# Optimization experiments

Hardware: AMD Instinct MI355X
Metric: run time of the kernel (lower is better)

Reference implementation:

```python
import jax, jax.numpy as jnp
import numpy as np

B, N, C, DK, TOPK = 4, 4096, 256, 64, 8


def setup_inputs() -> dict:
    key = jax.random.key(0)
    k1, k2, k3 = jax.random.split(key, 3)
    x = jax.random.normal(k1, (B, N, C), dtype=jnp.float32)
    # nn.Linear(channels, d_k, bias=False) weights, stored as [C, DK] for x @ W
    W_q = jax.random.normal(k2, (C, DK), dtype=jnp.float32) * (C ** -0.5)
    W_k = jax.random.normal(k3, (C, DK), dtype=jnp.float32) * (C ** -0.5)
    return {"x": x, "W_q": W_q, "W_k": W_k, "top_k": TOPK}


def reference(x, W_q, W_k, top_k):
    d_k = W_q.shape[-1]
    scale = d_k ** -0.5
    Q = x @ W_q                                   # [B, N, DK]
    K = x @ W_k                                   # [B, N, DK]
    S = jnp.einsum('bnd,bmd->bnm', Q, K) * scale  # [B, N, N]
    _, topk_idx = jax.lax.top_k(S, top_k)         # [B, N, top_k]
    n = S.shape[-1]
    # scatter True at top-k column indices per row (mirrors torch scatter_)
    row_mask = lambda idx: jnp.zeros((n,), dtype=bool).at[idx].set(True)
    mask = jax.vmap(jax.vmap(row_mask))(topk_idx)  # [B, N, N] bool
    S_masked = jnp.where(mask, S, -jnp.inf)
    A = jax.nn.softmax(S_masked, axis=-1)
    return A
```

## Files before the change

### kernel.cpp

```cpp
#include <hip/hip_runtime.h>
#include <math.h>

#define NROW 16384
#define NCOL 4096
#define CDIM 256
#define DKDIM 64
#define SCALE 0.125f

typedef float v4f __attribute__((ext_vector_type(4)));

__global__ __launch_bounds__(512, 2) void qk_proj(
    const float* __restrict__ x, const float* __restrict__ Wq,
    const float* __restrict__ Wk, float* __restrict__ Qt,
    float* __restrict__ Kt) {
  __shared__ float4 xs4[64][65];
  const int t = threadIdx.x;
  const int rb = blockIdx.x;
  {
    const float4* xg = (const float4*)(x + (size_t)rb * 64 * CDIM);
    #pragma unroll
    for (int i = 0; i < 8; ++i) {
      int idx = i * 512 + t;
      xs4[idx >> 6][idx & 63] = xg[idx];
    }
  }
  __syncthreads();

  const int lane = t & 63;
  const int wu = __builtin_amdgcn_readfirstlane(t >> 6);
  const int proj = wu >> 2;
  const int chunk = wu & 3;
  const float* __restrict__ Wp = proj ? Wk : Wq;

  float acc[16];
  #pragma unroll
  for (int j = 0; j < 16; ++j) acc[j] = 0.f;

  #pragma unroll 4
  for (int cs = 0; cs < 64; ++cs) {
    float4 xv = xs4[lane][cs];
    const float xc[4] = {xv.x, xv.y, xv.z, xv.w};
    #pragma unroll
    for (int i = 0; i < 4; ++i) {
      const float4* __restrict__ w4 =
          (const float4*)(Wp + (size_t)(cs * 4 + i) * DKDIM + chunk * 16);
      float4 wa = w4[0], wb = w4[1], wc = w4[2], wd = w4[3];
      float xi = xc[i];
      acc[0]  = fmaf(xi, wa.x, acc[0]);  acc[1]  = fmaf(xi, wa.y, acc[1]);
      acc[2]  = fmaf(xi, wa.z, acc[2]);  acc[3]  = fmaf(xi, wa.w, acc[3]);
      acc[4]  = fmaf(xi, wb.x, acc[4]);  acc[5]  = fmaf(xi, wb.y, acc[5]);
      acc[6]  = fmaf(xi, wb.z, acc[6]);  acc[7]  = fmaf(xi, wb.w, acc[7]);
      acc[8]  = fmaf(xi, wc.x, acc[8]);  acc[9]  = fmaf(xi, wc.y, acc[9]);
      acc[10] = fmaf(xi, wc.z, acc[10]); acc[11] = fmaf(xi, wc.w, acc[11]);
      acc[12] = fmaf(xi, wd.x, acc[12]); acc[13] = fmaf(xi, wd.y, acc[13]);
      acc[14] = fmaf(xi, wd.z, acc[14]); acc[15] = fmaf(xi, wd.w, acc[15]);
    }
  }

  const int gr = rb * 64 + lane;
  const int b = gr >> 12;
  const int n = gr & 4095;
  float4* __restrict__ Out4 = (float4*)(proj ? Kt : Qt);
  #pragma unroll
  for (int i = 0; i < 4; ++i) {
    int dg = chunk * 4 + i;
    float4 o = {acc[4 * i], acc[4 * i + 1], acc[4 * i + 2], acc[4 * i + 3]};
    Out4[(size_t)(b * 16 + dg) * 4096 + n] = o;
  }
}

__global__ __launch_bounds__(256, 4) void s_topk(
    const float* __restrict__ Qt, const float* __restrict__ Kt,
    float* __restrict__ out, float* __restrict__ wsv, int* __restrict__ wsi) {
  __shared__ float smem[8448];
  float4* qs = (float4*)smem;
  float (*cv)[33] = (float(*)[33])smem;
  int   (*ci)[33] = (int(*)[33])(smem + 128 * 33);

  const int t = threadIdx.x;
  const int f = blockIdx.x;
  const int slot = f & 7;
  const int i5 = f >> 3;
  const int cl = i5 >> 5;
  const int rbL = i5 & 31;
  const int combo = slot * 4 + cl;
  const int b = combo >> 3;
  const int chunk = combo & 7;
  const int lane = t & 63;
  const int wu = __builtin_amdgcn_readfirstlane(t >> 6);
  const int n0 = rbL * 128;

  const float4* __restrict__ Qt4 = (const float4*)Qt;
  #pragma unroll
  for (int i = 0; i < 8; ++i) {
    int idx = i * 256 + t;
    int g = idx >> 7, row = idx & 127;
    qs[g * 128 + row] = Qt4[(size_t)(b * 16 + g) * 4096 + n0 + row];
  }
  __syncthreads();

  {
    v4f z = {0.f, 0.f, 0.f, 0.f};
    v4f* o4 = (v4f*)out + (size_t)(b * 4096 + n0) * 1024 + chunk * 128;
    #pragma unroll 8
    for (int i = 0; i < 64; ++i) {
      int g = i * 256 + t;
      __builtin_nontemporal_store(z, &o4[(size_t)(g >> 7) * 1024 + (g & 127)]);
    }
  }

  const float4* __restrict__ Kt4 = (const float4*)Kt;
  const int stripe = chunk * 512 + wu * 128;

  float tv0[8], tv1[8]; int ti0[8], ti1[8];
  float tmin0, tmin1; int tmpos0, tmpos1;

  auto compute8 = [&](int cb, float* a0, float* a1) {
    #pragma unroll
    for (int j = 0; j < 8; ++j) { a0[j] = 0.f; a1[j] = 0.f; }
    #pragma unroll 2
    for (int g = 0; g < 16; ++g) {
      float4 qa = qs[g * 128 + lane];
      float4 qb = qs[g * 128 + 64 + lane];
      const float4* __restrict__ kg =
          Kt4 + (size_t)(b * 16 + g) * 4096 + cb;
      #pragma unroll
      for (int j = 0; j < 8; ++j) {
        float4 kf = kg[j];
        a0[j] = fmaf(qa.x, kf.x, a0[j]);
        a0[j] = fmaf(qa.y, kf.y, a0[j]);
        a0[j] = fmaf(qa.z, kf.z, a0[j]);
        a0[j] = fmaf(qa.w, kf.w, a0[j]);
        a1[j] = fmaf(qb.x, kf.x, a1[j]);
        a1[j] = fmaf(qb.y, kf.y, a1[j]);
        a1[j] = fmaf(qb.z, kf.z, a1[j]);
        a1[j] = fmaf(qb.w, kf.w, a1[j]);
      }
    }
  };

  auto update8 = [&](int cb, float* acc, float* tv, int* ti,
                     float& tmin, int& tmpos) {
    float bv = acc[0]; int bj = 0;
    #pragma unroll
    for (int j = 1; j < 8; ++j)
      if (acc[j] > bv) { bv = acc[j]; bj = j; }
    #pragma unroll
    for (int pass = 0; pass < 2; ++pass) {
      if (__any(bv > tmin)) {
        if (bv > tmin) {
          int col = cb + bj;
          #pragma unroll
          for (int q2 = 0; q2 < 8; ++q2)
            if (q2 == tmpos) { tv[q2] = bv; ti[q2] = col; }
          tmin = tv[0]; tmpos = 0;
          #pragma unroll
          for (int q2 = 1; q2 < 8; ++q2)
            if (tv[q2] < tmin) { tmin = tv[q2]; tmpos = q2; }
          #pragma unroll
          for (int j = 0; j < 8; ++j)
            if (j == bj) acc[j] = -INFINITY;
        }
        bv = acc[0]; bj = 0;
        #pragma unroll
        for (int j = 1; j < 8; ++j)
          if (acc[j] > bv) { bv = acc[j]; bj = j; }
      }
    }
    if (__any(bv > tmin)) {
      #pragma unroll
      for (int j = 0; j < 8; ++j) {
        float v = acc[j];
        if (v > tmin) {
          int col = cb + j;
          #pragma unroll
          for (int q2 = 0; q2 < 8; ++q2)
            if (q2 == tmpos) { tv[q2] = v; ti[q2] = col; }
          tmin = tv[0]; tmpos = 0;
          #pragma unroll
          for (int q2 = 1; q2 < 8; ++q2)
            if (tv[q2] < tmin) { tmin = tv[q2]; tmpos = q2; }
        }
      }
    }
  };

  {
    float a0[8], a1[8];
    compute8(stripe, a0, a1);
    #pragma unroll
    for (int j = 0; j < 8; ++j) {
      tv0[j] = a0[j]; ti0[j] = stripe + j;
      tv1[j] = a1[j]; ti1[j] = stripe + j;
    }
    tmin0 = tv0[0]; tmpos0 = 0; tmin1 = tv1[0]; tmpos1 = 0;
    #pragma unroll
    for (int q2 = 1; q2 < 8; ++q2) {
      if (tv0[q2] < tmin0) { tmin0 = tv0[q2]; tmpos0 = q2; }
      if (tv1[q2] < tmin1) { tmin1 = tv1[q2]; tmpos1 = q2; }
    }
  }

  #pragma unroll 1
  for (int cg = 1; cg < 16; ++cg) {
    const int cb = stripe + cg * 8;
    float a0[8], a1[8];
    compute8(cb, a0, a1);
    update8(cb, a0, tv0, ti0, tmin0, tmpos0);
    update8(cb, a1, tv1, ti1, tmin1, tmpos1);
  }

  __syncthreads();
  #pragma unroll
  for (int q2 = 0; q2 < 8; ++q2) {
    cv[lane][wu * 8 + q2] = tv0[q2];       ci[lane][wu * 8 + q2] = ti0[q2];
    cv[lane + 64][wu * 8 + q2] = tv1[q2];  ci[lane + 64][wu * 8 + q2] = ti1[q2];
  }
  __syncthreads();
  if (t < 128) {
    float rv[8]; int rid[8];
    #pragma unroll
    for (int q2 = 0; q2 < 8; ++q2) { rv[q2] = cv[t][q2]; rid[q2] = ci[t][q2]; }
    float m = rv[0]; int mp = 0;
    #pragma unroll
    for (int q2 = 1; q2 < 8; ++q2) if (rv[q2] < m) { m = rv[q2]; mp = q2; }
    #pragma unroll
    for (int c = 8; c < 32; ++c) {
      float v = cv[t][c];
      if (v > m) {
        int col = ci[t][c];
        #pragma unroll
        for (int q2 = 0; q2 < 8; ++q2) if (q2 == mp) { rv[q2] = v; rid[q2] = col; }
        m = rv[0]; mp = 0;
        #pragma unroll
        for (int q2 = 1; q2 < 8; ++q2) if (rv[q2] < m) { m = rv[q2]; mp = q2; }
      }
    }
    size_t gr = (size_t)(b * 4096 + n0) + t;
    #pragma unroll
    for (int q2 = 0; q2 < 8; ++q2) {
      wsv[gr * 64 + chunk * 8 + q2] = rv[q2];
      wsi[gr * 64 + chunk * 8 + q2] = rid[q2];
    }
  }
}

__global__ __launch_bounds__(256) void merge_scatter(
    const float* __restrict__ wsv, const int* __restrict__ wsi,
    float* __restrict__ out) {
  int row = blockIdx.x * 256 + threadIdx.x;
  const float4* v4 = (const float4*)(wsv + (size_t)row * 64);
  const int4*   i4 = (const int4*)(wsi + (size_t)row * 64);
  float rv[8]; int rid[8];
  {
    float4 a0 = v4[0], a1 = v4[1];
    int4   c0 = i4[0], c1 = i4[1];
    rv[0]=a0.x; rv[1]=a0.y; rv[2]=a0.z; rv[3]=a0.w;
    rv[4]=a1.x; rv[5]=a1.y; rv[6]=a1.z; rv[7]=a1.w;
    rid[0]=c0.x; rid[1]=c0.y; rid[2]=c0.z; rid[3]=c0.w;
    rid[4]=c1.x; rid[5]=c1.y; rid[6]=c1.z; rid[7]=c1.w;
  }
  float m = rv[0]; int mp = 0;
  #pragma unroll
  for (int q = 1; q < 8; ++q) if (rv[q] < m) { m = rv[q]; mp = q; }
  #pragma unroll 2
  for (int c4 = 2; c4 < 16; ++c4) {
    float4 a = v4[c4]; int4 ic = i4[c4];
    const float vv[4] = {a.x, a.y, a.z, a.w};
    const int   ii[4] = {ic.x, ic.y, ic.z, ic.w};
    #pragma unroll
    for (int k = 0; k < 4; ++k) {
      if (vv[k] > m) {
        #pragma unroll
        for (int q = 0; q < 8; ++q) if (q == mp) { rv[q] = vv[k]; rid[q] = ii[k]; }
        m = rv[0]; mp = 0;
        #pragma unroll
        for (int q = 1; q < 8; ++q) if (rv[q] < m) { m = rv[q]; mp = q; }
      }
    }
  }
  float vmax = rv[0];
  #pragma unroll
  for (int q = 1; q < 8; ++q) vmax = fmaxf(vmax, rv[q]);
  float e[8], s = 0.f;
  #pragma unroll
  for (int q = 0; q < 8; ++q) { e[q] = __expf((rv[q] - vmax) * SCALE); s += e[q]; }
  float inv = 1.f / s;
  float* orow = out + (size_t)row * NCOL;
  #pragma unroll
  for (int q = 0; q < 8; ++q) orow[rid[q]] = e[q] * inv;
}

extern "C" void kernel_launch(void* const* d_in, const int* in_sizes, int n_in,
                              void* d_out, int out_size, void* d_ws, size_t ws_size,
                              hipStream_t stream) {
  const float* x  = (const float*)d_in[0];
  const float* Wq = (const float*)d_in[1];
  const float* Wk = (const float*)d_in[2];
  float* out = (float*)d_out;

  char* ws = (char*)d_ws;
  float* Qt  = (float*)ws;
  float* Kt  = (float*)(ws + (size_t)NROW * DKDIM * 4);
  float* wsv = (float*)(ws + 2 * (size_t)NROW * DKDIM * 4);
  int*   wsi = (int*)  (ws + 2 * (size_t)NROW * DKDIM * 4 + (size_t)NROW * 64 * 4);

  qk_proj<<<dim3(NROW / 64), 512, 0, stream>>>(x, Wq, Wk, Qt, Kt);
  s_topk<<<1024, 256, 0, stream>>>(Qt, Kt, out, wsv, wsi);
  merge_scatter<<<NROW / 256, 256, 0, stream>>>(wsv, wsi, out);
}
```

Measured before the change: 546.8 us.

## Retile K layout, software-pipeline K loads, interleave zero-fill stores with compute

The K projection is now written in a blocked layout, grouping eight consecutive columns per dim-group so that each wave's K reads for a column group are contiguous. The s_topk inner loop keeps two K tiles of eight float4s loaded ahead in registers and fully unrolls the 16-group loop. The output zero-fill stores are spread across the column-group iterations so they overlap with compute instead of running up front. Launch bounds drop from 4 to 2 blocks per SM to make room for the extra registers, at the cost of occupancy.

```diff
diff --git a/kernel.cpp b/kernel.cpp
--- a/kernel.cpp
+++ b/kernel.cpp
@@ -60,16 +60,28 @@
   const int gr = rb * 64 + lane;
   const int b = gr >> 12;
   const int n = gr & 4095;
-  float4* __restrict__ Out4 = (float4*)(proj ? Kt : Qt);
-  #pragma unroll
-  for (int i = 0; i < 4; ++i) {
-    int dg = chunk * 4 + i;
-    float4 o = {acc[4 * i], acc[4 * i + 1], acc[4 * i + 2], acc[4 * i + 3]};
-    Out4[(size_t)(b * 16 + dg) * 4096 + n] = o;
+  if (proj == 0) {
+    float4* __restrict__ Out4 = (float4*)Qt;
+    #pragma unroll
+    for (int i = 0; i < 4; ++i) {
+      int dg = chunk * 4 + i;
+      float4 o = {acc[4 * i], acc[4 * i + 1], acc[4 * i + 2], acc[4 * i + 3]};
+      Out4[(size_t)(b * 16 + dg) * 4096 + n] = o;
+    }
+  } else {
+    float4* __restrict__ Out4 = (float4*)Kt;
+    #pragma unroll
+    for (int i = 0; i < 4; ++i) {
+      int dg = chunk * 4 + i;
+      float4 o = {acc[4 * i], acc[4 * i + 1], acc[4 * i + 2], acc[4 * i + 3]};
+      Out4[(((size_t)b * 512 + (n >> 3)) * 16 + dg) * 8 + (n & 7)] = o;
+    }
   }
 }
 
-__global__ __launch_bounds__(256, 4) void s_topk(
+struct K8 { float4 v[8]; };
+
+__global__ __launch_bounds__(256, 2) void s_topk(
     const float* __restrict__ Qt, const float* __restrict__ Kt,
     float* __restrict__ out, float* __restrict__ wsv, int* __restrict__ wsi) {
   __shared__ float smem[8448];
@@ -99,34 +111,39 @@
   }
   __syncthreads();
 
-  {
-    v4f z = {0.f, 0.f, 0.f, 0.f};
-    v4f* o4 = (v4f*)out + (size_t)(b * 4096 + n0) * 1024 + chunk * 128;
-    #pragma unroll 8
-    for (int i = 0; i < 64; ++i) {
-      int g = i * 256 + t;
-      __builtin_nontemporal_store(z, &o4[(size_t)(g >> 7) * 1024 + (g & 127)]);
-    }
-  }
-
   const float4* __restrict__ Kt4 = (const float4*)Kt;
   const int stripe = chunk * 512 + wu * 128;
+  const float4* __restrict__ Kb =
+      Kt4 + ((size_t)b * 512 + (stripe >> 3)) * 128;
+
+  v4f zfill = {0.f, 0.f, 0.f, 0.f};
+  v4f* o4 = (v4f*)out + (size_t)(b * 4096 + n0) * 1024 + chunk * 128;
 
   float tv0[8], tv1[8]; int ti0[8], ti1[8];
   float tmin0, tmin1; int tmpos0, tmpos1;
 
-  auto compute8 = [&](int cb, float* a0, float* a1) {
+  auto loadK = [&](const float4* p) {
+    K8 k;
+    #pragma unroll
+    for (int j = 0; j < 8; ++j) k.v[j] = p[j];
+    return k;
+  };
+
+  auto compute8 = [&](int cg, float* a0, float* a1) {
+    const float4* __restrict__ pc = Kb + (size_t)cg * 128;
     #pragma unroll
     for (int j = 0; j < 8; ++j) { a0[j] = 0.f; a1[j] = 0.f; }
-    #pragma unroll 2
+    K8 kA = loadK(pc);
+    K8 kB = loadK(pc + 8);
+    #pragma unroll
     for (int g = 0; g < 16; ++g) {
+      K8 kC;
+      if (g + 2 < 16) kC = loadK(pc + (size_t)(g + 2) * 8);
       float4 qa = qs[g * 128 + lane];
       float4 qb = qs[g * 128 + 64 + lane];
-      const float4* __restrict__ kg =
-          Kt4 + (size_t)(b * 16 + g) * 4096 + cb;
       #pragma unroll
       for (int j = 0; j < 8; ++j) {
-        float4 kf = kg[j];
+        float4 kf = kA.v[j];
         a0[j] = fmaf(qa.x, kf.x, a0[j]);
         a0[j] = fmaf(qa.y, kf.y, a0[j]);
         a0[j] = fmaf(qa.z, kf.z, a0[j]);
@@ -136,6 +153,8 @@
         a1[j] = fmaf(qb.z, kf.z, a1[j]);
         a1[j] = fmaf(qb.w, kf.w, a1[j]);
       }
+      kA = kB;
+      if (g + 2 < 16) kB = kC;
     }
   };
 
@@ -185,9 +204,18 @@
     }
   };
 
+  auto zstores = [&](int cg) {
+    #pragma unroll
+    for (int i = cg * 4; i < cg * 4 + 4; ++i) {
+      int g = i * 256 + t;
+      __builtin_nontemporal_store(zfill,
+          &o4[(size_t)(g >> 7) * 1024 + (g & 127)]);
+    }
+  };
+
   {
     float a0[8], a1[8];
-    compute8(stripe, a0, a1);
+    compute8(0, a0, a1);
     #pragma unroll
     for (int j = 0; j < 8; ++j) {
       tv0[j] = a0[j]; ti0[j] = stripe + j;
@@ -199,15 +227,17 @@
       if (tv0[q2] < tmin0) { tmin0 = tv0[q2]; tmpos0 = q2; }
       if (tv1[q2] < tmin1) { tmin1 = tv1[q2]; tmpos1 = q2; }
     }
+    zstores(0);
   }
 
   #pragma unroll 1
   for (int cg = 1; cg < 16; ++cg) {
     const int cb = stripe + cg * 8;
     float a0[8], a1[8];
-    compute8(cb, a0, a1);
+    compute8(cg, a0, a1);
     update8(cb, a0, tv0, ti0, tmin0, tmpos0);
     update8(cb, a1, tv1, ti1, tmin1, tmpos1);
+    zstores(cg);
   }
 
   __syncthreads();
```

Result: slower. 951.6 us (+74.0%).
